# Performance work log

Hardware: AMD Instinct MI355X
Metric: run time of the kernel (lower is better)

The kernel has to match this reference:

```python
import jax, jax.numpy as jnp
import numpy as np

N_NODES = 100000
N_EDGES = 1600000
N_GRAPHS = 512
HID = 192
EPS = 1e-5


def setup_inputs() -> dict:
    key = jax.random.key(0)
    ks = jax.random.split(key, 16)
    x = jax.random.normal(ks[0], (N_NODES, 1), dtype=jnp.float32)
    edge_index = jax.random.randint(ks[1], (2, N_EDGES), 0, N_NODES, dtype=jnp.int64)
    batch = jnp.sort(jax.random.randint(ks[2], (N_NODES,), 0, N_GRAPHS, dtype=jnp.int64))
    def lin(k, fi, fo):
        # torch nn.Linear default init: U(-1/sqrt(fi), 1/sqrt(fi))
        b = 1.0 / np.sqrt(fi)
        return jax.random.uniform(k, (fi, fo), jnp.float32, -b, b)
    return {
        "x": x, "edge_index": edge_index, "batch": batch,
        "W1": lin(ks[3], 1, HID), "b1": jnp.zeros((HID,), jnp.float32),
        "g1": jnp.ones((HID,), jnp.float32), "be1": jnp.zeros((HID,), jnp.float32), "a1": jnp.ones((HID,), jnp.float32),
        "W2": lin(ks[4], HID, HID), "b2": jnp.zeros((HID,), jnp.float32),
        "g2": jnp.ones((HID,), jnp.float32), "be2": jnp.zeros((HID,), jnp.float32), "a2": jnp.ones((HID,), jnp.float32),
        "Wc1": lin(ks[5], HID, HID // 2), "bc1": jax.random.uniform(ks[6], (HID // 2,), jnp.float32, -1/np.sqrt(HID), 1/np.sqrt(HID)),
        "Wc2": lin(ks[7], HID // 2, 4), "bc2": jax.random.uniform(ks[8], (4,), jnp.float32, -1/np.sqrt(HID // 2), 1/np.sqrt(HID // 2)),
    }


def gcn_conv(x, W, b, row, col, n):
    # PyG GCNConv: h = xW; add self-loops; norm = d^-1/2[src] * d^-1/2[dst]; scatter-add to dst; + bias
    h = x @ W
    sl = jnp.arange(n, dtype=row.dtype)
    r = jnp.concatenate([row, sl])
    c = jnp.concatenate([col, sl])
    deg = jax.ops.segment_sum(jnp.ones_like(c, dtype=h.dtype), c, num_segments=n)
    dinv = jnp.where(deg > 0, jax.lax.rsqrt(deg), 0.0)
    norm = dinv[r] * dinv[c]                      # [E+N]
    msg = h[r] * norm[:, None]                    # [E+N, HID] dominant gather
    return jax.ops.segment_sum(msg, c, num_segments=n) + b


def graph_norm(x, batch, gamma, beta, alpha, g):
    cnt = jax.ops.segment_sum(jnp.ones((x.shape[0],), x.dtype), batch, num_segments=g)
    cnt = jnp.maximum(cnt, 1.0)[:, None]
    mean = jax.ops.segment_sum(x, batch, num_segments=g) / cnt
    out = x - alpha * mean[batch]
    var = jax.ops.segment_sum(out * out, batch, num_segments=g) / cnt
    out = out * jax.lax.rsqrt(var + EPS)[batch]
    return gamma * out + beta


def reference(x, edge_index, batch, W1, b1, g1, be1, a1, W2, b2, g2, be2, a2, Wc1, bc1, Wc2, bc2):
    n = x.shape[0]
    row, col = edge_index[0], edge_index[1]
    h = gcn_conv(x, W1, b1, row, col, n)
    h = jax.nn.relu(graph_norm(h, batch, g1, be1, a1, N_GRAPHS))
    h = gcn_conv(h, W2, b2, row, col, n)
    h = jax.nn.relu(graph_norm(h, batch, g2, be2, a2, N_GRAPHS))
    # global mean pool (dropout is identity in eval mode)
    cnt = jnp.maximum(jax.ops.segment_sum(jnp.ones((n,), h.dtype), batch, num_segments=N_GRAPHS), 1.0)
    pooled = jax.ops.segment_sum(h, batch, num_segments=N_GRAPHS) / cnt[:, None]
    z = jax.nn.relu(pooled @ Wc1 + bc1)
    return z @ Wc2 + bc2
```

## Files before the change

### kernel.cpp

```cpp
#include <hip/hip_runtime.h>
#include <hip/hip_bf16.h>
#include <hip/hip_fp16.h>

#define N_NODES 100000
#define N_PAD 100032
#define N_EDGES 1600000
#define N_GRAPHS 512
#define HID 192
#define EPSV 1e-5f

using f16x8 = __attribute__((ext_vector_type(8))) _Float16;
using f16x4 = __attribute__((ext_vector_type(4))) _Float16;
using f32x4 = __attribute__((ext_vector_type(4))) float;

__global__ void k_count(const int* __restrict__ col, int* __restrict__ cnt) {
    int e = blockIdx.x * blockDim.x + threadIdx.x;
    if (e < N_EDGES) atomicAdd(&cnt[col[e]], 1);
}

__global__ void k_misc(const float* __restrict__ W2, _Float16* __restrict__ W2h,
                       const int* __restrict__ batch, int* __restrict__ gstart) {
    int id = blockIdx.x * blockDim.x + threadIdx.x;
    if (id < HID * HID) W2h[id] = (_Float16)W2[id];
    int g = id - HID * HID;
    if (g >= 0 && g <= N_GRAPHS) {
        if (g == N_GRAPHS) { gstart[g] = N_NODES; return; }
        int lo = 0, hi = N_NODES;
        while (lo < hi) { int mid = (lo + hi) >> 1; if (batch[mid] < g) lo = mid + 1; else hi = mid; }
        gstart[g] = lo;
    }
}

__global__ void k_scan_partial(const int* __restrict__ cnt, int* __restrict__ bsum) {
    __shared__ int sd[256];
    int base = blockIdx.x * 1024;
    int t = threadIdx.x;
    int s = 0;
    for (int j = 0; j < 4; ++j) {
        int i = base + j * 256 + t;
        if (i < N_NODES) s += cnt[i];
    }
    sd[t] = s; __syncthreads();
    for (int off = 128; off > 0; off >>= 1) {
        if (t < off) sd[t] += sd[t + off];
        __syncthreads();
    }
    if (t == 0) bsum[blockIdx.x] = sd[0];
}

__global__ void k_scan_final(const int* __restrict__ cnt, const int* __restrict__ bsum,
                             int nb, int* __restrict__ row_ptr, int* __restrict__ cur_acc,
                             float* __restrict__ dinv, const float* __restrict__ x,
                             float* __restrict__ xp) {
    __shared__ int sd[256];
    __shared__ int s_off;
    int bid = blockIdx.x;
    int t = threadIdx.x;
    int part = 0;
    for (int i = t; i < bid; i += 256) part += bsum[i];
    sd[t] = part; __syncthreads();
    for (int off = 128; off > 0; off >>= 1) {
        if (t < off) sd[t] += sd[t + off];
        __syncthreads();
    }
    if (t == 0) s_off = sd[0];
    __syncthreads();
    int base = bid * 1024;
    int idx0 = base + t * 4;
    int c[4]; int tot = 0;
    for (int j = 0; j < 4; ++j) {
        int i = idx0 + j;
        c[j] = (i < N_NODES) ? cnt[i] : 0;
        tot += c[j];
    }
    sd[t] = tot; __syncthreads();
    for (int off = 1; off < 256; off <<= 1) {
        int v = (t >= off) ? sd[t - off] : 0;
        __syncthreads();
        sd[t] += v;
        __syncthreads();
    }
    int excl = sd[t] - tot + s_off;
    for (int j = 0; j < 4; ++j) {
        int i = idx0 + j;
        if (i < N_NODES) {
            row_ptr[i] = excl;
            cur_acc[2 * i] = excl;
            cur_acc[2 * i + 1] = 0;
            float dv = rsqrtf((float)(c[j] + 1));
            dinv[i] = dv;
            xp[i] = x[i] * dv;
            excl += c[j];
        }
    }
    if (bid == nb - 1 && t == 255) row_ptr[N_NODES] = excl;
}

#define FILL_WIN 8
#define FILL_RANGE (N_NODES / FILL_WIN)
#define EPR ((N_EDGES + 255) / 256)
__global__ void __launch_bounds__(256) k_fill(const int* __restrict__ row,
                                              const int* __restrict__ col,
                                              const float* __restrict__ xp,
                                              int* __restrict__ cur_acc,
                                              int* __restrict__ csr_src) {
    int w = blockIdx.x & 7;
    int rank = blockIdx.x >> 3;
    int lo = w * FILL_RANGE;
    int hi = (w == FILL_WIN - 1) ? N_NODES : lo + FILL_RANGE;
    int e0 = rank * EPR;
    int e1 = min(e0 + EPR, N_EDGES);
    for (int e = e0 + threadIdx.x; e < e1; e += 256) {
        int c = col[e];
        if (c >= lo && c < hi) {
            int r = row[e];
            int pos = atomicAdd(&cur_acc[2 * c], 1);
            atomicAdd((float*)&cur_acc[2 * c + 1], xp[r]);
            csr_src[pos] = r;
        }
    }
}

__global__ void __launch_bounds__(192) k_stats_ab(const int* __restrict__ cur_acc,
                                                  const float* __restrict__ x,
                                                  const float* __restrict__ dinv,
                                                  const int* __restrict__ gstart,
                                                  const float* __restrict__ W1, const float* __restrict__ b1,
                                                  const float* __restrict__ g1, const float* __restrict__ be1,
                                                  const float* __restrict__ a1,
                                                  float* __restrict__ A, float* __restrict__ B) {
    __shared__ float sd[192], sd2[192];
    int g = blockIdx.x, t = threadIdx.x;
    int i0 = gstart[g], i1 = gstart[g + 1];
    const float* ca = (const float*)cur_acc;
    float s = 0.f, s2 = 0.f;
    for (int i = i0 + t; i < i1; i += 192) {
        float dv = dinv[i];
        float u = dv * (ca[2 * i + 1] + x[i] * dv);
        s += u; s2 += u * u;
    }
    sd[t] = s; sd2[t] = s2; __syncthreads();
    for (int off = 96; off >= 3; off >>= 1) {
        if (t < off) { sd[t] += sd[t + off]; sd2[t] += sd2[t + off]; }
        __syncthreads();
    }
    float sum_u = sd[0] + sd[1] + sd[2];
    float sum_u2 = sd2[0] + sd2[1] + sd2[2];
    float cntf = fmaxf((float)(i1 - i0), 1.f);
    float m = sum_u / cntf;
    float es2 = sum_u2 / cntf;
    int f = t;
    float w = W1[f], bb = b1[f], al = a1[f];
    float c2 = bb * (1.f - al);
    float d = al * m;
    float eud2 = es2 - 2.f * d * m + d * d;
    float var = w * w * eud2 + 2.f * w * c2 * (m - d) + c2 * c2;
    float rs = rsqrtf(var + EPSV);
    float gam = g1[f];
    A[g * HID + f] = gam * rs * w;
    B[g * HID + f] = gam * rs * (c2 - w * d) + be1[f];
}

__global__ void __launch_bounds__(256) k_x1(const int* __restrict__ cur_acc,
                                            const float* __restrict__ x,
                                            const float* __restrict__ dinv,
                                            const int* __restrict__ batch,
                                            const float* __restrict__ A,
                                            const float* __restrict__ B,
                                            _Float16* __restrict__ X1p) {
    int wid = threadIdx.x >> 6;
    int lane = threadIdx.x & 63;
    int v = blockIdx.x * 4 + wid;
    if (v >= N_NODES) return;
    float dv = dinv[v];
    float u = dv * (((const float*)cur_acc)[2 * v + 1] + x[v] * dv);
    int g = batch[v];
    int c4 = (lane < 48 ? lane : 47) * 4;
    float4 Av = *(const float4*)(A + g * HID + c4);
    float4 Bv = *(const float4*)(B + g * HID + c4);
    f16x4 o;
    o[0] = (_Float16)(fmaxf(fmaf(Av.x, u, Bv.x), 0.f) * dv);
    o[1] = (_Float16)(fmaxf(fmaf(Av.y, u, Bv.y), 0.f) * dv);
    o[2] = (_Float16)(fmaxf(fmaf(Av.z, u, Bv.z), 0.f) * dv);
    o[3] = (_Float16)(fmaxf(fmaf(Av.w, u, Bv.w), 0.f) * dv);
    if (lane < 48) *(f16x4*)(X1p + (size_t)v * HID + c4) = o;
}

#define CH 8
__global__ void __launch_bounds__(256) k_conv2(const _Float16* __restrict__ X1p,
                                               const float* __restrict__ dinv,
                                               const int* __restrict__ row_ptr,
                                               const int* __restrict__ csr_src,
                                               _Float16* __restrict__ aggh) {
    int wid = threadIdx.x >> 6;
    int lane = threadIdx.x & 63;
    int v = blockIdx.x * 4 + wid;
    if (v >= N_NODES) return;
    unsigned c8 = (unsigned)(lane < 48 ? lane : 47) * 8u;
    const char* Xb = (const char*)X1p;
    float dv = dinv[v];
    f16x4 sv = *(const f16x4*)(Xb + (unsigned)v * (HID * 2) + c8);
    float a0 = (float)sv[0], a1 = (float)sv[1], a2 = (float)sv[2], a3 = (float)sv[3];
    int e0 = row_ptr[v], e1 = row_ptr[v + 1];
    for (int b = e0; b < e1; b += CH) {
        unsigned off[CH]; float wgt[CH];
#pragma unroll
        for (int j = 0; j < CH; ++j) {
            int e = b + j;
            off[j] = (unsigned)csr_src[(e < e1) ? e : e0] * (unsigned)(HID * 2) + c8;
            wgt[j] = (e < e1) ? 1.f : 0.f;
        }
        f16x4 rv[CH];
#pragma unroll
        for (int j = 0; j < CH; ++j)
            rv[j] = *(const f16x4*)(Xb + off[j]);
#pragma unroll
        for (int j = 0; j < CH; ++j) {
            a0 = fmaf(wgt[j], (float)rv[j][0], a0);
            a1 = fmaf(wgt[j], (float)rv[j][1], a1);
            a2 = fmaf(wgt[j], (float)rv[j][2], a2);
            a3 = fmaf(wgt[j], (float)rv[j][3], a3);
        }
    }
    if (lane < 48) {
        f16x4 o;
        o[0] = (_Float16)(a0 * dv);
        o[1] = (_Float16)(a1 * dv);
        o[2] = (_Float16)(a2 * dv);
        o[3] = (_Float16)(a3 * dv);
        *(f16x4*)((char*)aggh + (unsigned)v * (HID * 2) + c8) = o;
    }
}

#define BM 64
__global__ void __launch_bounds__(256) k_gemm(const _Float16* __restrict__ A,
                                              const _Float16* __restrict__ W,
                                              const float* __restrict__ b2,
                                              const int* __restrict__ batch,
                                              _Float16* __restrict__ H,
                                              float* __restrict__ sums,
                                              float* __restrict__ sumsq) {
    __shared__ _Float16 a_lds[BM * HID];
    __shared__ int bb[BM];
    int t = threadIdx.x;
    int wid = t >> 6, lane = t & 63;
    int row0 = blockIdx.x * BM;
    if (t < BM) { int gr = row0 + t; bb[t] = (gr < N_NODES) ? batch[gr] : -1; }
    const char* Ablk = (const char*)(A + (size_t)row0 * HID);
#pragma unroll
    for (int it = 0; it < 6; ++it) {
        int bo = (it * 256 + t) * 16;
        int r = bo / 384;
        int swz = bo ^ ((r & 7) << 4);
        *(float4*)((char*)a_lds + swz) = *(const float4*)(Ablk + bo);
    }
    int n0 = wid * 48;
    int bn = n0 + (lane & 15);
    int bk0 = (lane >> 4) << 3;
    f16x8 bfr[6][3];
#pragma unroll
    for (int kc = 0; kc < 6; ++kc)
#pragma unroll
        for (int nt = 0; nt < 3; ++nt) {
            const _Float16* src = W + (size_t)(kc * 32 + bk0) * HID + bn + nt * 16;
            f16x8 v;
#pragma unroll
            for (int j = 0; j < 8; ++j) v[j] = src[(size_t)j * HID];
            bfr[kc][nt] = v;
        }
    __syncthreads();
    f32x4 acc[4][3];
#pragma unroll
    for (int mt = 0; mt < 4; ++mt)
#pragma unroll
        for (int nt = 0; nt < 3; ++nt) acc[mt][nt] = (f32x4){0.f, 0.f, 0.f, 0.f};
    int ar = lane & 15;
#pragma unroll
    for (int mt = 0; mt < 4; ++mt) {
        int r = mt * 16 + ar;
        int rbase = r * 384;
        int sw = (r & 7) << 4;
#pragma unroll
        for (int kc = 0; kc < 6; ++kc) {
            int bo = (rbase + (kc * 32 + bk0) * 2) ^ sw;
            f16x8 a = *(const f16x8*)((const char*)a_lds + bo);
            acc[mt][0] = __builtin_amdgcn_mfma_f32_16x16x32_f16(a, bfr[kc][0], acc[mt][0], 0, 0, 0);
            acc[mt][1] = __builtin_amdgcn_mfma_f32_16x16x32_f16(a, bfr[kc][1], acc[mt][1], 0, 0, 0);
            acc[mt][2] = __builtin_amdgcn_mfma_f32_16x16x32_f16(a, bfr[kc][2], acc[mt][2], 0, 0, 0);
        }
    }
    int cn = lane & 15;
    int rb = (lane >> 4) * 4;
    float bias[3];
#pragma unroll
    for (int nt = 0; nt < 3; ++nt) bias[nt] = b2[n0 + nt * 16 + cn];
    int gA = bb[0];
    int lastv = min(BM, N_NODES - row0) - 1;
    int gB = bb[lastv];
    float sA[3] = {0.f,0.f,0.f}, qA[3] = {0.f,0.f,0.f};
    float sB[3] = {0.f,0.f,0.f}, qB[3] = {0.f,0.f,0.f};
#pragma unroll
    for (int mt = 0; mt < 4; ++mt)
#pragma unroll
        for (int r = 0; r < 4; ++r) {
            int ridx = mt * 16 + rb + r;
            int grow = row0 + ridx;
            if (grow < N_NODES) {
                int gi = bb[ridx];
                _Float16* o = H + (size_t)grow * HID;
#pragma unroll
                for (int nt = 0; nt < 3; ++nt) {
                    float val = acc[mt][nt][r] + bias[nt];
                    o[n0 + nt * 16 + cn] = (_Float16)val;
                    if (gi == gA) { sA[nt] += val; qA[nt] += val * val; }
                    else          { sB[nt] += val; qB[nt] += val * val; }
                }
            }
        }
#pragma unroll
    for (int nt = 0; nt < 3; ++nt) {
        sA[nt] += __shfl_xor(sA[nt], 16); sA[nt] += __shfl_xor(sA[nt], 32);
        qA[nt] += __shfl_xor(qA[nt], 16); qA[nt] += __shfl_xor(qA[nt], 32);
        sB[nt] += __shfl_xor(sB[nt], 16); sB[nt] += __shfl_xor(sB[nt], 32);
        qB[nt] += __shfl_xor(qB[nt], 16); qB[nt] += __shfl_xor(qB[nt], 32);
    }
    if (lane < 16) {
#pragma unroll
        for (int nt = 0; nt < 3; ++nt) {
            int colf = n0 + nt * 16 + cn;
            atomicAdd(&sums[gA * HID + colf], sA[nt]);
            atomicAdd(&sumsq[gA * HID + colf], qA[nt]);
            if (gB != gA) {
                atomicAdd(&sums[gB * HID + colf], sB[nt]);
                atomicAdd(&sumsq[gB * HID + colf], qB[nt]);
            }
        }
    }
}

__global__ void __launch_bounds__(192) k_pool(const _Float16* __restrict__ h,
                                              const int* __restrict__ batch,
                                              const int* __restrict__ gstart,
                                              const float* __restrict__ sums,
                                              const float* __restrict__ sumsq,
                                              const float* __restrict__ g2,
                                              const float* __restrict__ be2,
                                              const float* __restrict__ a2,
                                              float* __restrict__ pooled) {
    int f = threadIdx.x;
    int r0 = blockIdx.x * 64;
    int r1 = min(r0 + 64, N_NODES);
    float al = a2[f], gam = g2[f], bet = be2[f];
    int g = batch[r0];
    float Cg, Dg;
    auto cd = [&](int gg) {
        float cntf = fmaxf((float)(gstart[gg + 1] - gstart[gg]), 1.f);
        float mh = sums[gg * HID + f] / cntf;
        float msq = sumsq[gg * HID + f] / cntf;
        float var = msq - 2.f * al * mh * mh + al * al * mh * mh;
        Cg = gam * rsqrtf(var + EPSV);
        Dg = bet - Cg * al * mh;
    };
    cd(g);
    float s = 0.f;
    int i = r0;
    for (; i + 4 <= r1; i += 4) {
        int g0 = batch[i], g3 = batch[i + 3];
        float v0 = (float)h[(size_t)(i + 0) * HID + f];
        float v1 = (float)h[(size_t)(i + 1) * HID + f];
        float v2 = (float)h[(size_t)(i + 2) * HID + f];
        float v3 = (float)h[(size_t)(i + 3) * HID + f];
        if (g0 == g && g3 == g) {
            s += fmaxf(fmaf(Cg, v0, Dg), 0.f) + fmaxf(fmaf(Cg, v1, Dg), 0.f);
            s += fmaxf(fmaf(Cg, v2, Dg), 0.f) + fmaxf(fmaf(Cg, v3, Dg), 0.f);
        } else {
            float vv[4] = {v0, v1, v2, v3};
            for (int j = 0; j < 4; ++j) {
                int gi = batch[i + j];
                if (gi != g) {
                    atomicAdd(&pooled[g * HID + f], s);
                    s = 0.f; g = gi; cd(g);
                }
                s += fmaxf(fmaf(Cg, vv[j], Dg), 0.f);
            }
        }
    }
    for (; i < r1; ++i) {
        int gi = batch[i];
        float v = (float)h[(size_t)i * HID + f];
        if (gi != g) {
            atomicAdd(&pooled[g * HID + f], s);
            s = 0.f; g = gi; cd(g);
        }
        s += fmaxf(fmaf(Cg, v, Dg), 0.f);
    }
    atomicAdd(&pooled[g * HID + f], s);
}

__global__ void __launch_bounds__(128) k_mlp(const float* __restrict__ pooled,
                                             const int* __restrict__ gstart,
                                             const float* __restrict__ Wc1,
                                             const float* __restrict__ bc1,
                                             const float* __restrict__ Wc2,
                                             const float* __restrict__ bc2,
                                             float* __restrict__ out) {
    __shared__ float p[HID];
    __shared__ float z[96];
    int g = blockIdx.x, t = threadIdx.x;
    float inv = 1.f / fmaxf((float)(gstart[g + 1] - gstart[g]), 1.f);
    for (int i = t; i < HID; i += 128) p[i] = pooled[g * HID + i] * inv;
    __syncthreads();
    if (t < 96) {
        float acc = bc1[t];
        for (int k = 0; k < HID; ++k) acc += p[k] * Wc1[k * 96 + t];
        z[t] = fmaxf(acc, 0.f);
    }
    __syncthreads();
    if (t < 4) {
        float acc = bc2[t];
        for (int j = 0; j < 96; ++j) acc += z[j] * Wc2[j * 4 + t];
        out[g * 4 + t] = acc;
    }
}

extern "C" void kernel_launch(void* const* d_in, const int* in_sizes, int n_in,
                              void* d_out, int out_size, void* d_ws, size_t ws_size,
                              hipStream_t stream) {
    const float* x   = (const float*)d_in[0];
    const int* eidx  = (const int*)d_in[1];
    const int* batch = (const int*)d_in[2];
    const float* W1  = (const float*)d_in[3];
    const float* b1  = (const float*)d_in[4];
    const float* g1  = (const float*)d_in[5];
    const float* be1 = (const float*)d_in[6];
    const float* a1  = (const float*)d_in[7];
    const float* W2  = (const float*)d_in[8];
    const float* b2  = (const float*)d_in[9];
    const float* g2  = (const float*)d_in[10];
    const float* be2 = (const float*)d_in[11];
    const float* a2  = (const float*)d_in[12];
    const float* Wc1 = (const float*)d_in[13];
    const float* bc1 = (const float*)d_in[14];
    const float* Wc2 = (const float*)d_in[15];
    const float* bc2 = (const float*)d_in[16];
    const int* row = eidx;
    const int* col = eidx + N_EDGES;
    float* out = (float*)d_out;

    char* ws = (char*)d_ws;
    size_t off = 0;
    auto alloc = [&](size_t bytes) -> char* {
        char* p = ws + off;
        off = (off + bytes + 255) & ~(size_t)255;
        return p;
    };
    int*   cnt     = (int*)  alloc(N_NODES * 4);
    float* sums2   = (float*)alloc(N_GRAPHS * HID * 4);
    float* sumsq2  = (float*)alloc(N_GRAPHS * HID * 4);
    float* pooled  = (float*)alloc(N_GRAPHS * HID * 4);
    size_t zbytes  = off;
    int*   bsum    = (int*)  alloc(128 * 4);
    int*   row_ptr = (int*)  alloc((N_NODES + 1) * 4);
    int*   cur_acc = (int*)  alloc((size_t)N_NODES * 8);
    int*   csr_src = (int*)  alloc(N_EDGES * 4);
    float* dinv    = (float*)alloc(N_NODES * 4);
    float* xp      = (float*)alloc(N_NODES * 4);
    float* Atab    = (float*)alloc(N_GRAPHS * HID * 4);
    float* Btab    = (float*)alloc(N_GRAPHS * HID * 4);
    int*   gstart  = (int*)  alloc((N_GRAPHS + 1) * 4);
    _Float16* X1p  = (_Float16*)alloc((size_t)N_NODES * HID * 2);
    _Float16* aggh = (_Float16*)alloc((size_t)N_PAD * HID * 2);
    _Float16* h2   = (_Float16*)alloc((size_t)N_NODES * HID * 2);
    _Float16* W2h  = (_Float16*)alloc((size_t)HID * HID * 2);

    hipMemsetAsync(ws, 0, zbytes, stream);
    k_misc<<<(HID * HID + N_GRAPHS + 1 + 255) / 256, 256, 0, stream>>>(W2, W2h, batch, gstart);
    k_count<<<(N_EDGES + 255) / 256, 256, 0, stream>>>(col, cnt);
    int PB = (N_NODES + 1023) / 1024;
    k_scan_partial<<<PB, 256, 0, stream>>>(cnt, bsum);
    k_scan_final<<<PB, 256, 0, stream>>>(cnt, bsum, PB, row_ptr, cur_acc, dinv, x, xp);
    k_fill<<<2048, 256, 0, stream>>>(row, col, xp, cur_acc, csr_src);
    k_stats_ab<<<N_GRAPHS, 192, 0, stream>>>(cur_acc, x, dinv, gstart, W1, b1, g1, be1, a1, Atab, Btab);
    k_x1<<<(N_NODES + 3) / 4, 256, 0, stream>>>(cur_acc, x, dinv, batch, Atab, Btab, X1p);
    k_conv2<<<(N_NODES + 3) / 4, 256, 0, stream>>>(X1p, dinv, row_ptr, csr_src, aggh);
    k_gemm<<<(N_NODES + BM - 1) / BM, 256, 0, stream>>>(aggh, W2h, b2, batch, h2, sums2, sumsq2);
    int SB = (N_NODES + 63) / 64;
    k_pool<<<SB, 192, 0, stream>>>(h2, batch, gstart, sums2, sumsq2, g2, be2, a2, pooled);
    k_mlp<<<N_GRAPHS, 128, 0, stream>>>(pooled, gstart, Wc1, bc1, Wc2, bc2, out);
}
```

Baseline: 400.6 us.

## Replace float atomic layer-1 aggregation with CSR gather and packed node info

Removes the per-edge float atomicAdd of xp[r] from the CSR fill kernel, leaving only the cursor atomic. The layer-1 scalar aggregation now runs in a new pull-style kernel that walks each node's CSR row, gathers xp in batches of 16, and writes u, dinv and the graph id into one packed float4 per node. The stats and x1 kernels then read that single float4 instead of several separate arrays. This adds a kernel launch and a second pass over csr_src with random xp gathers, in exchange for removing 1.6M contended float atomics.

```diff
diff --git a/kernel.cpp b/kernel.cpp
--- a/kernel.cpp
+++ b/kernel.cpp
@@ -49,7 +49,7 @@
 }
 
 __global__ void k_scan_final(const int* __restrict__ cnt, const int* __restrict__ bsum,
-                             int nb, int* __restrict__ row_ptr, int* __restrict__ cur_acc,
+                             int nb, int* __restrict__ row_ptr, int* __restrict__ cursor,
                              float* __restrict__ dinv, const float* __restrict__ x,
                              float* __restrict__ xp) {
     __shared__ int sd[256];
@@ -85,8 +85,7 @@
         int i = idx0 + j;
         if (i < N_NODES) {
             row_ptr[i] = excl;
-            cur_acc[2 * i] = excl;
-            cur_acc[2 * i + 1] = 0;
+            cursor[i] = excl;
             float dv = rsqrtf((float)(c[j] + 1));
             dinv[i] = dv;
             xp[i] = x[i] * dv;
@@ -101,8 +100,7 @@
 #define EPR ((N_EDGES + 255) / 256)
 __global__ void __launch_bounds__(256) k_fill(const int* __restrict__ row,
                                               const int* __restrict__ col,
-                                              const float* __restrict__ xp,
-                                              int* __restrict__ cur_acc,
+                                              int* __restrict__ cursor,
                                               int* __restrict__ csr_src) {
     int w = blockIdx.x & 7;
     int rank = blockIdx.x >> 3;
@@ -113,17 +111,35 @@
     for (int e = e0 + threadIdx.x; e < e1; e += 256) {
         int c = col[e];
         if (c >= lo && c < hi) {
-            int r = row[e];
-            int pos = atomicAdd(&cur_acc[2 * c], 1);
-            atomicAdd((float*)&cur_acc[2 * c + 1], xp[r]);
-            csr_src[pos] = r;
-        }
-    }
-}
-
-__global__ void __launch_bounds__(192) k_stats_ab(const int* __restrict__ cur_acc,
-                                                  const float* __restrict__ x,
-                                                  const float* __restrict__ dinv,
+            int pos = atomicAdd(&cursor[c], 1);
+            csr_src[pos] = row[e];
+        }
+    }
+}
+
+__global__ void k_layer1(const float* __restrict__ x, const float* __restrict__ xp,
+                         const int* __restrict__ batch,
+                         const int* __restrict__ row_ptr, const int* __restrict__ csr_src,
+                         const float* __restrict__ dinv, float4* __restrict__ node_info) {
+    int v = blockIdx.x * blockDim.x + threadIdx.x;
+    if (v >= N_NODES) return;
+    int e0 = row_ptr[v], e1 = row_ptr[v + 1];
+    float acc = 0.f;
+    for (int base = e0; base < e1; base += 16) {
+        int src[16]; float xv[16];
+#pragma unroll
+        for (int j = 0; j < 16; ++j) { int e = base + j; src[j] = csr_src[(e < e1) ? e : e0]; }
+#pragma unroll
+        for (int j = 0; j < 16; ++j) { xv[j] = xp[src[j]]; }
+#pragma unroll
+        for (int j = 0; j < 16; ++j) { acc += (base + j < e1) ? xv[j] : 0.f; }
+    }
+    float dv = dinv[v];
+    float u = dv * acc + x[v] * dv * dv;
+    node_info[v] = make_float4(u, dv, __int_as_float((int)batch[v]), 0.f);
+}
+
+__global__ void __launch_bounds__(192) k_stats_ab(const float4* __restrict__ node_info,
                                                   const int* __restrict__ gstart,
                                                   const float* __restrict__ W1, const float* __restrict__ b1,
                                                   const float* __restrict__ g1, const float* __restrict__ be1,
@@ -132,13 +148,8 @@
     __shared__ float sd[192], sd2[192];
     int g = blockIdx.x, t = threadIdx.x;
     int i0 = gstart[g], i1 = gstart[g + 1];
-    const float* ca = (const float*)cur_acc;
     float s = 0.f, s2 = 0.f;
-    for (int i = i0 + t; i < i1; i += 192) {
-        float dv = dinv[i];
-        float u = dv * (ca[2 * i + 1] + x[i] * dv);
-        s += u; s2 += u * u;
-    }
+    for (int i = i0 + t; i < i1; i += 192) { float u = node_info[i].x; s += u; s2 += u * u; }
     sd[t] = s; sd2[t] = s2; __syncthreads();
     for (int off = 96; off >= 3; off >>= 1) {
         if (t < off) { sd[t] += sd[t + off]; sd2[t] += sd2[t + off]; }
@@ -161,10 +172,7 @@
     B[g * HID + f] = gam * rs * (c2 - w * d) + be1[f];
 }
 
-__global__ void __launch_bounds__(256) k_x1(const int* __restrict__ cur_acc,
-                                            const float* __restrict__ x,
-                                            const float* __restrict__ dinv,
-                                            const int* __restrict__ batch,
+__global__ void __launch_bounds__(256) k_x1(const float4* __restrict__ node_info,
                                             const float* __restrict__ A,
                                             const float* __restrict__ B,
                                             _Float16* __restrict__ X1p) {
@@ -172,9 +180,9 @@
     int lane = threadIdx.x & 63;
     int v = blockIdx.x * 4 + wid;
     if (v >= N_NODES) return;
-    float dv = dinv[v];
-    float u = dv * (((const float*)cur_acc)[2 * v + 1] + x[v] * dv);
-    int g = batch[v];
+    float4 ni = node_info[v];
+    float u = ni.x, dv = ni.y;
+    int g = __float_as_int(ni.z);
     int c4 = (lane < 48 ? lane : 47) * 4;
     float4 Av = *(const float4*)(A + g * HID + c4);
     float4 Bv = *(const float4*)(B + g * HID + c4);
@@ -461,10 +469,11 @@
     size_t zbytes  = off;
     int*   bsum    = (int*)  alloc(128 * 4);
     int*   row_ptr = (int*)  alloc((N_NODES + 1) * 4);
-    int*   cur_acc = (int*)  alloc((size_t)N_NODES * 8);
+    int*   cursor  = (int*)  alloc(N_NODES * 4);
     int*   csr_src = (int*)  alloc(N_EDGES * 4);
     float* dinv    = (float*)alloc(N_NODES * 4);
     float* xp      = (float*)alloc(N_NODES * 4);
+    float4* node_info = (float4*)alloc((size_t)N_NODES * 16);
     float* Atab    = (float*)alloc(N_GRAPHS * HID * 4);
     float* Btab    = (float*)alloc(N_GRAPHS * HID * 4);
     int*   gstart  = (int*)  alloc((N_GRAPHS + 1) * 4);
@@ -478,10 +487,11 @@
     k_count<<<(N_EDGES + 255) / 256, 256, 0, stream>>>(col, cnt);
     int PB = (N_NODES + 1023) / 1024;
     k_scan_partial<<<PB, 256, 0, stream>>>(cnt, bsum);
-    k_scan_final<<<PB, 256, 0, stream>>>(cnt, bsum, PB, row_ptr, cur_acc, dinv, x, xp);
-    k_fill<<<2048, 256, 0, stream>>>(row, col, xp, cur_acc, csr_src);
-    k_stats_ab<<<N_GRAPHS, 192, 0, stream>>>(cur_acc, x, dinv, gstart, W1, b1, g1, be1, a1, Atab, Btab);
-    k_x1<<<(N_NODES + 3) / 4, 256, 0, stream>>>(cur_acc, x, dinv, batch, Atab, Btab, X1p);
+    k_scan_final<<<PB, 256, 0, stream>>>(cnt, bsum, PB, row_ptr, cursor, dinv, x, xp);
+    k_fill<<<2048, 256, 0, stream>>>(row, col, cursor, csr_src);
+    k_layer1<<<(N_NODES + 255) / 256, 256, 0, stream>>>(x, xp, batch, row_ptr, csr_src, dinv, node_info);
+    k_stats_ab<<<N_GRAPHS, 192, 0, stream>>>(node_info, gstart, W1, b1, g1, be1, a1, Atab, Btab);
+    k_x1<<<(N_NODES + 3) / 4, 256, 0, stream>>>(node_info, Atab, Btab, X1p);
     k_conv2<<<(N_NODES + 3) / 4, 256, 0, stream>>>(X1p, dinv, row_ptr, csr_src, aggh);
     k_gemm<<<(N_NODES + BM - 1) / BM, 256, 0, stream>>>(aggh, W2h, b2, batch, h2, sums2, sumsq2);
     int SB = (N_NODES + 63) / 64;
```

New measurement: 337.0 us (median of 3 runs). 15.9% less time.
